# Kernel tuning notes

Hardware: AMD Instinct MI355X
Metric: run time of the kernel (lower is better)

Reference implementation:

```python
import jax, jax.numpy as jnp
import numpy as np

EPS = 1e-5  # BatchNorm2d eps
NEG_SLOPE = 0.01  # LeakyReLU default


def _cconv_bn_act(x, W, b, g, beta):
    # Complex 1x1 conv + per-part BatchNorm (batch stats) + LeakyReLU.
    # x: [B,2,C,F,T]; W: [2,C,C] (real, imag); b, g, beta: [2,C]
    xr, xi = x[:, 0], x[:, 1]
    yr = (jnp.einsum('oc,bcft->boft', W[0], xr)
          - jnp.einsum('oc,bcft->boft', W[1], xi) + b[0][None, :, None, None])
    yi = (jnp.einsum('oc,bcft->boft', W[0], xi)
          + jnp.einsum('oc,bcft->boft', W[1], xr) + b[1][None, :, None, None])

    def bn(y, gg, bb):
        mu = y.mean(axis=(0, 2, 3), keepdims=True)
        var = y.var(axis=(0, 2, 3), keepdims=True)  # biased, as torch BN normalization
        return (y - mu) / jnp.sqrt(var + EPS) * gg[None, :, None, None] + bb[None, :, None, None]

    yr = jax.nn.leaky_relu(bn(yr, g[0], beta[0]), NEG_SLOPE)
    yi = jax.nn.leaky_relu(bn(yi, g[1], beta[1]), NEG_SLOPE)
    return jnp.stack((yr, yi), axis=1)


def _complex_attn(q, k, v):
    # q,k,v: [B,2,N,D]; magnitude-based scores, softmax over dim=1 of [B,N,N]
    # (faithful to nn.Softmax(dim=1) applied to a 3-D score tensor).
    qr, qi = q[:, 0], q[:, 1]
    kr, ki = k[:, 0], k[:, 1]
    sr = jnp.einsum('bnd,bmd->bnm', qr, kr) + jnp.einsum('bnd,bmd->bnm', qi, ki)
    si = jnp.einsum('bnd,bmd->bnm', qi, kr) - jnp.einsum('bnd,bmd->bnm', qr, ki)
    a = jax.nn.softmax(jnp.sqrt(sr * sr + si * si), axis=1)
    outr = jnp.einsum('bnm,bmd->bnd', a, v[:, 0])
    outi = jnp.einsum('bnm,bmd->bnd', a, v[:, 1])
    return jnp.stack((outr, outi), axis=1)


def _forward(P, Q, W, b, g, beta):
    B, _, C, F, T = P.shape
    # --- Time-axis attention: tokens = T frames, feature dim = C*F ---
    qt = _cconv_bn_act(Q, W[0], b[0], g[0], beta[0])
    kt = _cconv_bn_act(P, W[1], b[1], g[1], beta[1])
    vt = _cconv_bn_act(P, W[2], b[2], g[2], beta[2])

    def to_time(x):  # [B,2,C,F,T] -> [B,2,T,C*F]
        return x.reshape(B, 2, C * F, T).transpose(0, 1, 3, 2)

    ot = _complex_attn(to_time(qt), to_time(kt), to_time(vt))
    ot = ot.transpose(0, 1, 3, 2).reshape(B, 2, C, F, T)

    # --- Freq-axis attention: tokens = F bins, feature dim = C*T ---
    qf = _cconv_bn_act(Q, W[3], b[3], g[3], beta[3])
    kf = _cconv_bn_act(P, W[4], b[4], g[4], beta[4])
    vf = _cconv_bn_act(P, W[5], b[5], g[5], beta[5])

    def to_freq(x):  # [B,2,C,F,T] -> [B,2,F,C*T]
        return x.transpose(0, 1, 3, 2, 4).reshape(B, 2, F, C * T)

    of = _complex_attn(to_freq(qf), to_freq(kf), to_freq(vf))
    of = of.reshape(B, 2, F, C, T).transpose(0, 1, 3, 2, 4)

    # Combine the two attention axes (truncated top-level module; see notes).
    return ot + of


def setup_inputs():
    key = jax.random.key(0)
    ks = jax.random.split(key, 4)
    B, C, F, T = 2, 64, 256, 256
    P = jax.random.normal(ks[0], (B, 2, C, F, T), dtype=jnp.float32)
    Q = jax.random.normal(ks[1], (B, 2, C, F, T), dtype=jnp.float32)
    # 6 branches: [time-q, time-k, time-v, freq-q, freq-k, freq-v]
    W = jax.random.normal(ks[2], (6, 2, C, C), dtype=jnp.float32) / np.sqrt(C).astype(np.float32)
    b = jax.random.normal(ks[3], (6, 2, C), dtype=jnp.float32) * 0.01
    g = jnp.ones((6, 2, C), dtype=jnp.float32)
    beta = jnp.zeros((6, 2, C), dtype=jnp.float32)
    return {"P": P, "Q": Q, "W": W, "b": b, "g": g, "beta": beta}


def reference(P, Q, W, b, g, beta):
    return _forward(P, Q, W, b, g, beta)
```

## Files before the change

kernel.cpp:

```cpp
#include <hip/hip_runtime.h>
#include <math.h>

#define SS 65536
#define PLANE 4194304
#define TEN_ELEMS 16777216
#define NSAMP 131072.0f

typedef __bf16 bf16x8 __attribute__((ext_vector_type(8)));
typedef __bf16 bf16x4v __attribute__((ext_vector_type(4)));
typedef float  f32x4  __attribute__((ext_vector_type(4)));

__device__ inline f32x4 mfma16(bf16x8 a, bf16x8 b, f32x4 c) {
  return __builtin_amdgcn_mfma_f32_16x16x32_bf16(a, b, c, 0, 0, 0);
}
__device__ inline bf16x8 neg8(bf16x8 v) {
  union { bf16x8 b; unsigned u[4]; } t; t.b = v;
#pragma unroll
  for (int i = 0; i < 4; ++i) t.u[i] ^= 0x80008000u;
  return t.b;
}
__device__ inline float bnlrelu(float v, float sc, float sh) {
  float t = fmaf(v, sc, sh);
  return t > 0.f ? t : 0.01f * t;
}

__device__ inline int swz(int r, int g) {
  return r * 40 + (((g ^ (r >> 2) ^ (r >> 4)) & 3) << 3);
}

__global__ __launch_bounds__(256) void stats_cov(
    const float* __restrict__ xQ, const float* __restrict__ xP,
    float* __restrict__ cpart, float* __restrict__ mbuck)
{
  __shared__ __align__(16) __bf16 sXh[128 * 72];
  __shared__ __align__(16) __bf16 sXl[128 * 72];
  const int tid = threadIdx.x;
  const int win = blockIdx.x;
  const int tz = blockIdx.y;
  const float* x = tz ? xP : xQ;
  const int w = tid >> 6, q = (tid >> 4) & 3, ln = tid & 15;
  const int pcb = tid >> 4;
  const int s4 = (tid & 15) * 4;

  f32x4 zero = {0.f, 0.f, 0.f, 0.f};
  f32x4 acc[2][8];
#pragma unroll
  for (int mt = 0; mt < 2; ++mt)
#pragma unroll
    for (int nt = 0; nt < 8; ++nt) acc[mt][nt] = zero;
  float msum[8] = {0.f, 0.f, 0.f, 0.f, 0.f, 0.f, 0.f, 0.f};

  for (int half = 0; half < 8; ++half) {
    const int bb = half >> 2;
    const int sbase = win * 256 + (half & 3) * 64;
#pragma unroll
    for (int r = 0; r < 8; ++r) {
      int pc = pcb + r * 16;
      float4 v4 = *(const float4*)&x[(size_t)(bb * 128 + pc) * SS + sbase + s4];
      msum[r] += v4.x + v4.y + v4.z + v4.w;
      float vv[4] = {v4.x, v4.y, v4.z, v4.w};
      bf16x4v hv, lv;
#pragma unroll
      for (int e = 0; e < 4; ++e) {
        __bf16 h = (__bf16)vv[e];
        hv[e] = h; lv[e] = (__bf16)(vv[e] - (float)h);
      }
      *(bf16x4v*)&sXh[pc * 72 + s4] = hv;
      *(bf16x4v*)&sXl[pc * 72 + s4] = lv;
    }
    __syncthreads();
#pragma unroll
    for (int ks = 0; ks < 2; ++ks) {
      bf16x8 ah[2], al[2];
#pragma unroll
      for (int mt = 0; mt < 2; ++mt) {
        int ra = w * 32 + mt * 16 + ln;
        ah[mt] = *(const bf16x8*)&sXh[ra * 72 + ks * 32 + q * 8];
        al[mt] = *(const bf16x8*)&sXl[ra * 72 + ks * 32 + q * 8];
      }
#pragma unroll
      for (int nt = 0; nt < 8; ++nt) {
        int rb = nt * 16 + ln;
        bf16x8 bh = *(const bf16x8*)&sXh[rb * 72 + ks * 32 + q * 8];
        bf16x8 bl = *(const bf16x8*)&sXl[rb * 72 + ks * 32 + q * 8];
#pragma unroll
        for (int mt = 0; mt < 2; ++mt) {
          f32x4 a = acc[mt][nt];
          a = mfma16(ah[mt], bh, a);
          a = mfma16(ah[mt], bl, a);
          a = mfma16(al[mt], bh, a);
          acc[mt][nt] = a;
        }
      }
    }
    __syncthreads();
  }
#pragma unroll
  for (int r = 0; r < 8; ++r) {
    float v = msum[r];
#pragma unroll
    for (int off = 1; off < 16; off <<= 1) v += __shfl_xor(v, off, 64);
    if (ln == 0)
      atomicAdd(&mbuck[((win & 63) * 2 + tz) * 128 + pcb + r * 16], v);
  }
  float* cp = cpart + ((size_t)tz * 256 + win) * 16384;
#pragma unroll
  for (int mt = 0; mt < 2; ++mt)
#pragma unroll
    for (int nt = 0; nt < 8; ++nt)
#pragma unroll
      for (int r = 0; r < 4; ++r) {
        int row = w * 32 + mt * 16 + q * 4 + r;
        int col = nt * 16 + ln;
        cp[row * 128 + col] = acc[mt][nt][r];
      }
}

__global__ __launch_bounds__(256) void cov_reduce(
    const float* __restrict__ cpart, const float* __restrict__ mbuck,
    float* __restrict__ csum, float* __restrict__ msum)
{
  int i = blockIdx.x * 256 + threadIdx.x;
  int tz = i >> 14, e = i & 16383;
  const float* p = cpart + (size_t)tz * 256 * 16384 + e;
  float s = 0.f;
#pragma unroll 4
  for (int k = 0; k < 256; ++k) s += p[(size_t)k * 16384];
  csum[i] = s;
  if (i < 256) {
    int t2 = i >> 7, row = i & 127;
    float sm2 = 0.f;
#pragma unroll 4
    for (int k = 0; k < 64; ++k) sm2 += mbuck[(k * 2 + t2) * 128 + row];
    msum[i] = sm2;
  }
}

__global__ void bn_precompute(
    const float* __restrict__ Cq, const float* __restrict__ Cp,
    const float* __restrict__ mq, const float* __restrict__ mp,
    const float* __restrict__ W, const float* __restrict__ g,
    const float* __restrict__ beta,
    float* __restrict__ scale6, float* __restrict__ shift6)
{
  const int rr = blockIdx.x >> 7;
  const int o  = blockIdx.x & 127;
  const int i  = threadIdx.x;
  const float* C = (rr % 3 == 0) ? Cq : Cp;
  const float* m = (rr % 3 == 0) ? mq : mp;
  const int po = o >> 6, co = o & 63;
  const int pi = i >> 6, ci = i & 63;
  float wv = W[rr * 8192 + ((po ^ pi) << 12) + co * 64 + ci];
  if (po == 0 && pi == 1) wv = -wv;
  __shared__ float sW[128];
  sW[i] = wv;
  __syncthreads();
  float t = 0.f;
  const float* crow = C + i * 128;
#pragma unroll 8
  for (int j = 0; j < 128; ++j) t += crow[j] * sW[j];
  float pv = wv * t;
  float pm = wv * m[i];
#pragma unroll
  for (int off = 1; off < 64; off <<= 1) {
    pv += __shfl_xor(pv, off, 64);
    pm += __shfl_xor(pm, off, 64);
  }
  __shared__ float red[4];
  if ((i & 63) == 0) { red[(i >> 6) * 2] = pv; red[(i >> 6) * 2 + 1] = pm; }
  __syncthreads();
  if (i == 0) {
    float v = red[0] + red[2];
    float wm = red[1] + red[3];
    float muT = wm / NSAMP;
    float var = v / NSAMP - muT * muT;
    float sc = g[rr * 128 + o] * rsqrtf(var + 1e-5f);
    scale6[rr * 128 + o] = sc;
    shift6[rr * 128 + o] = beta[rr * 128 + o] - muT * sc;
  }
}

__global__ __launch_bounds__(256) void cconv_mfma(
    const float* __restrict__ x, const float* __restrict__ Wj,
    const float* __restrict__ scale, const float* __restrict__ shiftp,
    void* __restrict__ outA, void* __restrict__ outB, int mode, int freq)
{
  __shared__ __align__(16) char smemBlk[34816];
  __bf16* sBh = (__bf16*)smemBlk;
  __bf16* sBl = (__bf16*)(smemBlk + 17408);
  const int tid = threadIdx.x;
  const int b = blockIdx.y;
  const int s0 = blockIdx.x << 6;
  const int w = tid >> 6, q = (tid >> 4) & 3, ln = tid & 15;

  bf16x8 ah[2][4], al[2][4];
#pragma unroll
  for (int mt = 0; mt < 2; ++mt) {
    int row = w * 32 + mt * 16 + ln;
    int po = row >> 6, co = row & 63;
#pragma unroll
    for (int ks = 0; ks < 4; ++ks) {
      bf16x8 vh, vl;
#pragma unroll
      for (int j = 0; j < 8; ++j) {
        int k = ks * 32 + q * 8 + j;
        int pi = k >> 6, c = k & 63;
        float v = Wj[((po ^ pi) << 12) + co * 64 + c];
        if (po == 0 && pi == 1) v = -v;
        __bf16 h = (__bf16)v;
        vh[j] = h;
        vl[j] = (__bf16)(v - (float)h);
      }
      ah[mt][ks] = vh; al[mt][ks] = vl;
    }
  }

#pragma unroll
  for (int ph = 0; ph < 2; ++ph) {
    int pc = ph * 64 + (tid & 63);
    const float* rowp = x + (size_t)(b * 128 + pc) * SS + s0;
#pragma unroll
    for (int sh2 = 0; sh2 < 2; ++sh2)
#pragma unroll
      for (int sc2 = 0; sc2 < 2; ++sc2) {
        int sl = ((tid >> 6) << 3) + sh2 * 32 + sc2 * 4;
        float4 rd = *(const float4*)&rowp[sl];
        float vv[4] = {rd.x, rd.y, rd.z, rd.w};
#pragma unroll
        for (int e = 0; e < 4; ++e) {
          __bf16 h = (__bf16)vv[e];
          sBh[(sl + e) * 136 + pc] = h;
          sBl[(sl + e) * 136 + pc] = (__bf16)(vv[e] - (float)h);
        }
      }
  }
  __syncthreads();

  f32x4 zero = {0.f, 0.f, 0.f, 0.f};
  f32x4 acc[2][4];
#pragma unroll
  for (int mt = 0; mt < 2; ++mt)
#pragma unroll
    for (int nt = 0; nt < 4; ++nt) acc[mt][nt] = zero;

#pragma unroll
  for (int ks = 0; ks < 4; ++ks) {
    bf16x8 bh[4], bl[4];
#pragma unroll
    for (int nt = 0; nt < 4; ++nt) {
      int off = (nt * 16 + ln) * 136 + ks * 32 + q * 8;
      bh[nt] = *(const bf16x8*)&sBh[off];
      bl[nt] = *(const bf16x8*)&sBl[off];
    }
#pragma unroll
    for (int mt = 0; mt < 2; ++mt)
#pragma unroll
      for (int nt = 0; nt < 4; ++nt) {
        acc[mt][nt] = mfma16(ah[mt][ks], bh[nt], acc[mt][nt]);
        acc[mt][nt] = mfma16(ah[mt][ks], bl[nt], acc[mt][nt]);
        acc[mt][nt] = mfma16(al[mt][ks], bh[nt], acc[mt][nt]);
      }
  }

  float scv[2][4], shv[2][4];
#pragma unroll
  for (int mt = 0; mt < 2; ++mt)
#pragma unroll
    for (int r = 0; r < 4; ++r) {
      int row = w * 32 + mt * 16 + q * 4 + r;
      scv[mt][r] = scale[row];
      shv[mt][r] = shiftp[row];
    }

  if (mode == 2) {
    float* y = (float*)outA;
#pragma unroll
    for (int mt = 0; mt < 2; ++mt)
#pragma unroll
      for (int r = 0; r < 4; ++r) {
        int row = w * 32 + mt * 16 + q * 4 + r;
#pragma unroll
        for (int nt = 0; nt < 4; ++nt)
          y[(size_t)(b * 128 + row) * SS + s0 + nt * 16 + ln] =
              bnlrelu(acc[mt][nt][r], scv[mt][r], shv[mt][r]);
      }
  } else if (mode == 1) {
    __bf16* vh = (__bf16*)outA;
    __bf16* vl = (__bf16*)outB;
    const int f = s0 >> 8, t0 = s0 & 255;
#pragma unroll
    for (int mt = 0; mt < 2; ++mt)
#pragma unroll
      for (int r = 0; r < 4; ++r) {
        int row = w * 32 + mt * 16 + q * 4 + r;
        int p = row >> 6, c = row & 63;
        size_t rbase = ((size_t)((b * 2 + p) * 16384 + c * 256 + f)) * 256 + t0;
#pragma unroll
        for (int nt = 0; nt < 4; ++nt) {
          float v = bnlrelu(acc[mt][nt][r], scv[mt][r], shv[mt][r]);
          __bf16 h = (__bf16)v;
          vh[rbase + nt * 16 + ln] = h;
          vl[rbase + nt * 16 + ln] = (__bf16)(v - (float)h);
        }
      }
  } else {
    __syncthreads();
    float* sT = (float*)smemBlk;
#pragma unroll
    for (int mt = 0; mt < 2; ++mt)
#pragma unroll
      for (int nt = 0; nt < 4; ++nt)
#pragma unroll
        for (int r = 0; r < 4; ++r)
          sT[(nt * 16 + ln) * 133 + (w * 32 + mt * 16 + q * 4 + r)] =
              bnlrelu(acc[mt][nt][r], scv[mt][r], shv[mt][r]);
    __syncthreads();
    const int pch = tid >> 6, tl = tid & 63;
    float vv[32];
#pragma unroll
    for (int j2 = 0; j2 < 8; ++j2)
      *(f32x4*)&vv[j2 * 4] = *(const f32x4*)&sT[tl * 133 + pch * 32 + j2 * 4];
    bf16x8 hh[4], ll[4];
#pragma unroll
    for (int j2 = 0; j2 < 4; ++j2)
#pragma unroll
      for (int e = 0; e < 8; ++e) {
        float v = vv[j2 * 8 + e];
        __bf16 h = (__bf16)v;
        hh[j2][e] = h; ll[j2][e] = (__bf16)(v - (float)h);
      }
    __bf16* out = (__bf16*)outA;
    if (!freq) {
      const int p = pch >> 1, ch2 = pch & 1;
      int chunk = (s0 >> 8) * 2 + ch2;
      int tok = (s0 & 255) + tl;
      size_t a = (size_t)(b * 2 + p) * (2 * (size_t)PLANE) +
                 ((size_t)chunk * 256 + tok) * 64;
#pragma unroll
      for (int j2 = 0; j2 < 4; ++j2) {
        *(bf16x8*)&out[a + j2 * 8]      = hh[j2];
        *(bf16x8*)&out[a + 32 + j2 * 8] = ll[j2];
      }
    } else {
      __syncthreads();
      __bf16* sP = (__bf16*)smemBlk;
      __bf16* me = sP + tid * 64;
#pragma unroll
      for (int j2 = 0; j2 < 4; ++j2) {
        *(bf16x8*)&me[j2 * 8]      = hh[j2];
        *(bf16x8*)&me[32 + j2 * 8] = ll[j2];
      }
      __syncthreads();
#pragma unroll
      for (int r2 = 0; r2 < 8; ++r2) {
        int u = tid + (r2 << 8);
        int g2 = u >> 3, piece = u & 7;
        int pch2 = g2 >> 6, t2 = g2 & 63;
        int chunk = ((s0 & 255) + t2) * 2 + (pch2 & 1);
        int tok = s0 >> 8;
        size_t a = (size_t)(b * 2 + (pch2 >> 1)) * (2 * (size_t)PLANE) +
                   ((size_t)chunk * 256 + tok) * 64 + piece * 8;
        *(bf16x8*)&out[a] = *(const bf16x8*)&sP[(size_t)u * 8];
      }
    }
  }
}

__global__ __launch_bounds__(256) void score_mfma(
    const __bf16* __restrict__ qt, const __bf16* __restrict__ kt,
    float* __restrict__ SR, float* __restrict__ SI)
{
  __shared__ __align__(16) __bf16 sQh[2 * 128 * 40], sQl[2 * 128 * 40];
  __shared__ __align__(16) __bf16 sKh[2 * 64 * 40],  sKl[2 * 64 * 40];
  const int tid = threadIdx.x;
  const int sid = blockIdx.x + (blockIdx.y << 3) + (blockIdx.z << 8);
  const int kk = sid & 7, tt = sid >> 3;
  const int n0 = (kk & 1) << 7;
  const int b  = (kk >> 1) & 1;
  const int m0 = (tt & 3) << 6;
  const int g0 = (((kk >> 2) << 4) + (tt >> 2)) << 4;
  const int w = tid >> 6, q4 = (tid >> 4) & 3, ln = tid & 15;
  const size_t pb = (size_t)(b * 2) * (2 * (size_t)PLANE);

  f32x4 zero = {0.f, 0.f, 0.f, 0.f};
  f32x4 accr[2][4], acci[2][4];
#pragma unroll
  for (int st = 0; st < 2; ++st)
#pragma unroll
    for (int mt = 0; mt < 4; ++mt) { accr[st][mt] = zero; acci[st][mt] = zero; }

  for (int ch = 0; ch < 16; ++ch) {
    const int g = g0 + ch;
    const int Gq = g * 256 + n0;
    const int Gk = g * 256 + m0;
#pragma unroll
    for (int r = 0; r < 4; ++r) {
      int u = tid + (r << 8);
      int g_ = u & 3, tok = (u >> 2) & 127, p = u >> 9;
      size_t a = pb + (size_t)p * (2 * (size_t)PLANE) +
                 (size_t)(Gq + tok) * 64 + (g_ << 3);
      int dst = swz(p * 128 + tok, g_);
      *(bf16x8*)&sQh[dst] = *(const bf16x8*)&qt[a];
      *(bf16x8*)&sQl[dst] = *(const bf16x8*)&qt[a + 32];
    }
#pragma unroll
    for (int r = 0; r < 2; ++r) {
      int u = tid + (r << 8);
      int g_ = u & 3, tok = (u >> 2) & 63, p = u >> 8;
      size_t a = pb + (size_t)p * (2 * (size_t)PLANE) +
                 (size_t)(Gk + tok) * 64 + (g_ << 3);
      int dst = swz(p * 64 + tok, g_);
      *(bf16x8*)&sKh[dst] = *(const bf16x8*)&kt[a];
      *(bf16x8*)&sKl[dst] = *(const bf16x8*)&kt[a + 32];
    }
    __syncthreads();

    bf16x8 qh[2][2], ql2[2][2], nqh[2], nql[2];
#pragma unroll
    for (int st = 0; st < 2; ++st) {
      int tokn = w * 32 + st * 16 + ln;
#pragma unroll
      for (int p = 0; p < 2; ++p) {
        int off = swz(p * 128 + tokn, q4);
        qh[st][p]  = *(const bf16x8*)&sQh[off];
        ql2[st][p] = *(const bf16x8*)&sQl[off];
      }
      nqh[st] = neg8(qh[st][0]);
      nql[st] = neg8(ql2[st][0]);
    }
#pragma unroll
    for (int mt = 0; mt < 4; ++mt) {
      int tk = mt * 16 + ln;
      int offr = swz(tk, q4), offi = swz(64 + tk, q4);
      bf16x8 krh = *(const bf16x8*)&sKh[offr];
      bf16x8 krl = *(const bf16x8*)&sKl[offr];
      bf16x8 kih = *(const bf16x8*)&sKh[offi];
      bf16x8 kil = *(const bf16x8*)&sKl[offi];
#pragma unroll
      for (int st = 0; st < 2; ++st) {
        f32x4 ar = accr[st][mt], ai = acci[st][mt];
        ar = mfma16(qh[st][0], krh, ar);
        ar = mfma16(qh[st][0], krl, ar);
        ar = mfma16(ql2[st][0], krh, ar);
        ar = mfma16(qh[st][1], kih, ar);
        ar = mfma16(qh[st][1], kil, ar);
        ar = mfma16(ql2[st][1], kih, ar);
        ai = mfma16(qh[st][1], krh, ai);
        ai = mfma16(qh[st][1], krl, ai);
        ai = mfma16(ql2[st][1], krh, ai);
        ai = mfma16(nqh[st], kih, ai);
        ai = mfma16(nqh[st], kil, ai);
        ai = mfma16(nql[st], kih, ai);
        accr[st][mt] = ar; acci[st][mt] = ai;
      }
    }
    __syncthreads();
  }

#pragma unroll
  for (int st = 0; st < 2; ++st)
#pragma unroll
    for (int mt = 0; mt < 4; ++mt)
#pragma unroll
      for (int r = 0; r < 4; ++r) {
        int n = n0 + w * 32 + st * 16 + q4 * 4 + r;
        int m = m0 + mt * 16 + ln;
        int idx = (b << 16) + (n << 8) + m;
        atomicAdd(&SR[idx], accr[st][mt][r]);
        atomicAdd(&SI[idx], acci[st][mt][r]);
      }
}

__global__ __launch_bounds__(256) void softmax_kernel(
    const float* __restrict__ sr, const float* __restrict__ si,
    float* __restrict__ am)
{
  const int m = blockIdx.x & 255;
  const int b = blockIdx.x >> 8;
  const int n = threadIdx.x;
  const int idx = (b << 16) + (n << 8) + m;
  float vr = sr[idx], vi = si[idx];
  float mag = sqrtf(vr * vr + vi * vi);
  __shared__ float wmax[4];
  __shared__ float wsum[4];
  float mx = mag;
  #pragma unroll
  for (int off = 1; off < 64; off <<= 1)
    mx = fmaxf(mx, __shfl_xor(mx, off, 64));
  if ((threadIdx.x & 63) == 0) wmax[threadIdx.x >> 6] = mx;
  __syncthreads();
  mx = fmaxf(fmaxf(wmax[0], wmax[1]), fmaxf(wmax[2], wmax[3]));
  float e = expf(mag - mx);
  float sm = e;
  #pragma unroll
  for (int off = 1; off < 64; off <<= 1)
    sm += __shfl_xor(sm, off, 64);
  if ((threadIdx.x & 63) == 0) wsum[threadIdx.x >> 6] = sm;
  __syncthreads();
  float tot = wsum[0] + wsum[1] + wsum[2] + wsum[3];
  am[idx] = e / tot;
}

__global__ __launch_bounds__(256) void vt_transpose(
    const float* __restrict__ y2, __bf16* __restrict__ vh,
    __bf16* __restrict__ vl)
{
  __shared__ float sT[64 * 65];
  const int tid = threadIdx.x;
  const int bpc = blockIdx.y;
  const int bp = bpc >> 6, c = bpc & 63;
  const int f0 = (blockIdx.x >> 2) << 6, t0 = (blockIdx.x & 3) << 6;
  const float* src = y2 + (size_t)bp * PLANE + (size_t)c * SS;
#pragma unroll
  for (int r = 0; r < 4; ++r) {
    int fl = (tid >> 4) + (r << 4);
    int tl = (tid & 15) << 2;
    float4 v = *(const float4*)&src[(f0 + fl) * 256 + t0 + tl];
    sT[fl * 65 + tl + 0] = v.x;
    sT[fl * 65 + tl + 1] = v.y;
    sT[fl * 65 + tl + 2] = v.z;
    sT[fl * 65 + tl + 3] = v.w;
  }
  __syncthreads();
  __bf16* dsth = vh + (((size_t)bp * 16384 + c * 256) << 8);
  __bf16* dstl = vl + (((size_t)bp * 16384 + c * 256) << 8);
#pragma unroll
  for (int r = 0; r < 4; ++r) {
    int tl = (tid >> 4) + (r << 4);
    int fl = (tid & 15) << 2;
    bf16x4v h, l;
#pragma unroll
    for (int e = 0; e < 4; ++e) {
      float vv = sT[(fl + e) * 65 + tl];
      __bf16 hh = (__bf16)vv;
      h[e] = hh; l[e] = (__bf16)(vv - (float)hh);
    }
    *(bf16x4v*)&dsth[(size_t)(t0 + tl) * 256 + f0 + fl] = h;
    *(bf16x4v*)&dstl[(size_t)(t0 + tl) * 256 + f0 + fl] = l;
  }
}

__global__ __launch_bounds__(256) void av_mfma(
    const float* __restrict__ am, const __bf16* __restrict__ vth,
    const __bf16* __restrict__ vtl, float* __restrict__ out, int freq)
{
  __shared__ __align__(16) char smem[55296];
  __bf16* sVh = (__bf16*)smem;
  __bf16* sVl = (__bf16*)(smem + 18432);
  __bf16* sAh = (__bf16*)(smem + 36864);
  __bf16* sAl = (__bf16*)(smem + 46080);
  const int tid = threadIdx.x;
  const int d0 = blockIdx.x << 7;
  const int n0 = blockIdx.y << 6;
  const int bp = blockIdx.z, b = bp >> 1;
  const int w = tid >> 6, q = (tid >> 4) & 3, ln = tid & 15;
  const __bf16* vhp = vth + (((size_t)bp * 16384 + d0) << 8);
  const __bf16* vlp = vtl + (((size_t)bp * 16384 + d0) << 8);
  float* op = out + (size_t)bp * PLANE;

  f32x4 zero = {0.f, 0.f, 0.f, 0.f};
  f32x4 acc[2][4];
#pragma unroll
  for (int mt = 0; mt < 2; ++mt)
#pragma unroll
    for (int nt = 0; nt < 4; ++nt) acc[mt][nt] = zero;

  for (int m0 = 0; m0 < 256; m0 += 64) {
#pragma unroll
    for (int r = 0; r < 4; ++r) {
      int u = tid + (r << 8);
      int dl = u >> 3, g = (u & 7) << 3;
      *(bf16x8*)&sVh[dl * 72 + g] = *(const bf16x8*)&vhp[dl * 256 + m0 + g];
      *(bf16x8*)&sVl[dl * 72 + g] = *(const bf16x8*)&vlp[dl * 256 + m0 + g];
    }
#pragma unroll
    for (int r = 0; r < 4; ++r) {
      int u = tid + (r << 8);
      int mj = (u & 15) << 2, nl = u >> 4;
      float4 v4 = *(const float4*)&am[(b << 16) + ((n0 + nl) << 8) + m0 + mj];
      float vv[4] = {v4.x, v4.y, v4.z, v4.w};
      bf16x4v h, l;
#pragma unroll
      for (int e = 0; e < 4; ++e) {
        __bf16 hh = (__bf16)vv[e];
        h[e] = hh; l[e] = (__bf16)(vv[e] - (float)hh);
      }
      *(bf16x4v*)&sAh[nl * 72 + mj] = h;
      *(bf16x4v*)&sAl[nl * 72 + mj] = l;
    }
    __syncthreads();

#pragma unroll
    for (int ks = 0; ks < 2; ++ks) {
      bf16x8 vhf[2], vlf[2], ahf[4], alf[4];
#pragma unroll
      for (int mt = 0; mt < 2; ++mt) {
        int off = (w * 32 + mt * 16 + ln) * 72 + ks * 32 + q * 8;
        vhf[mt] = *(const bf16x8*)&sVh[off];
        vlf[mt] = *(const bf16x8*)&sVl[off];
      }
#pragma unroll
      for (int nt = 0; nt < 4; ++nt) {
        int off = (nt * 16 + ln) * 72 + ks * 32 + q * 8;
        ahf[nt] = *(const bf16x8*)&sAh[off];
        alf[nt] = *(const bf16x8*)&sAl[off];
      }
#pragma unroll
      for (int mt = 0; mt < 2; ++mt)
#pragma unroll
        for (int nt = 0; nt < 4; ++nt) {
          f32x4 a = acc[mt][nt];
          a = mfma16(vhf[mt], ahf[nt], a);
          a = mfma16(vhf[mt], alf[nt], a);
          a = mfma16(vlf[mt], ahf[nt], a);
          acc[mt][nt] = a;
        }
    }
    __syncthreads();
  }

  if (!freq) {
#pragma unroll
    for (int mt = 0; mt < 2; ++mt)
#pragma unroll
      for (int nt = 0; nt < 4; ++nt)
#pragma unroll
        for (int r = 0; r < 4; ++r) {
          int row = d0 + w * 32 + mt * 16 + q * 4 + r;
          op[(size_t)row * 256 + n0 + nt * 16 + ln] = acc[mt][nt][r];
        }
  } else {
    float* sO = (float*)smem;
#pragma unroll
    for (int mt = 0; mt < 2; ++mt)
#pragma unroll
      for (int nt = 0; nt < 4; ++nt)
#pragma unroll
        for (int r = 0; r < 4; ++r)
          sO[(w * 32 + mt * 16 + q * 4 + r) * 65 + nt * 16 + ln] = acc[mt][nt][r];
    __syncthreads();
    const int c = d0 >> 8, t0 = d0 & 255;
    const int dl = (tid & 31) << 2, nb = tid >> 5;
#pragma unroll
    for (int r = 0; r < 8; ++r) {
      int n = nb + (r << 3);
      float4 wv = make_float4(sO[(dl + 0) * 65 + n], sO[(dl + 1) * 65 + n],
                              sO[(dl + 2) * 65 + n], sO[(dl + 3) * 65 + n]);
      size_t addr = (size_t)c * SS + (size_t)(n0 + n) * 256 + t0 + dl;
      float4 o = *(float4*)&op[addr];
      wv.x += o.x; wv.y += o.y; wv.z += o.z; wv.w += o.w;
      *(float4*)&op[addr] = wv;
    }
  }
}

extern "C" void kernel_launch(void* const* d_in, const int* in_sizes, int n_in,
                              void* d_out, int out_size, void* d_ws, size_t ws_size,
                              hipStream_t stream) {
  const float* P    = (const float*)d_in[0];
  const float* Q    = (const float*)d_in[1];
  const float* W    = (const float*)d_in[2];
  const float* g    = (const float*)d_in[4];
  const float* beta = (const float*)d_in[5];
  float* out = (float*)d_out;
  float* ws  = (float*)d_ws;

  float* Y0    = ws;
  float* Y1    = Y0 + TEN_ELEMS;
  float* Y2    = Y1 + TEN_ELEMS;
  float* SR    = Y2 + TEN_ELEMS;
  float* SI    = SR + 131072;
  float* AM    = SI + 131072;
  float* MBUCK = AM + 131072;
  float* CSUM  = MBUCK + 16384;
  float* MSUM  = CSUM + 32768;
  float* SCALE6 = MSUM + 256;
  float* SHIFT6 = SCALE6 + 768;

  hipMemsetAsync(MBUCK, 0, 16384 * sizeof(float), stream);
  stats_cov<<<dim3(256, 2), 256, 0, stream>>>(Q, P, Y2, MBUCK);
  cov_reduce<<<128, 256, 0, stream>>>(Y2, MBUCK, CSUM, MSUM);
  bn_precompute<<<768, 128, 0, stream>>>(CSUM, CSUM + 16384, MSUM, MSUM + 128,
                                         W, g, beta, SCALE6, SHIFT6);

  for (int phase = 0; phase < 2; ++phase) {
    int j0 = phase * 3;
    int freq = phase;
    cconv_mfma<<<dim3(1024, 2), 256, 0, stream>>>(
        Q, W + (size_t)j0 * 8192, SCALE6 + j0 * 128, SHIFT6 + j0 * 128,
        Y0, nullptr, 0, freq);
    cconv_mfma<<<dim3(1024, 2), 256, 0, stream>>>(
        P, W + (size_t)(j0 + 1) * 8192, SCALE6 + (j0 + 1) * 128,
        SHIFT6 + (j0 + 1) * 128, Y1, nullptr, 0, freq);
    if (!freq)
      cconv_mfma<<<dim3(1024, 2), 256, 0, stream>>>(
          P, W + (size_t)(j0 + 2) * 8192, SCALE6 + (j0 + 2) * 128,
          SHIFT6 + (j0 + 2) * 128, Y2, (char*)Y2 + (size_t)TEN_ELEMS * 2, 1, 0);
    else
      cconv_mfma<<<dim3(1024, 2), 256, 0, stream>>>(
          P, W + (size_t)(j0 + 2) * 8192, SCALE6 + (j0 + 2) * 128,
          SHIFT6 + (j0 + 2) * 128, Y2, nullptr, 2, 1);

    hipMemsetAsync(SR, 0, 2 * 131072 * sizeof(float), stream);
    score_mfma<<<dim3(8, 32, 2), 256, 0, stream>>>(
        (const __bf16*)Y0, (const __bf16*)Y1, SR, SI);
    softmax_kernel<<<512, 256, 0, stream>>>(SR, SI, AM);

    const __bf16* VTh;
    const __bf16* VTl;
    if (!freq) {
      VTh = (const __bf16*)Y2;
      VTl = (const __bf16*)((char*)Y2 + (size_t)TEN_ELEMS * 2);
    } else {
      vt_transpose<<<dim3(16, 256), 256, 0, stream>>>(
          Y2, (__bf16*)Y0, (__bf16*)((char*)Y0 + (size_t)TEN_ELEMS * 2));
      VTh = (const __bf16*)Y0;
      VTl = (const __bf16*)((char*)Y0 + (size_t)TEN_ELEMS * 2);
    }
    av_mfma<<<dim3(128, 4, 4), 256, 0, stream>>>(AM, VTh, VTl, out, freq);
  }
}
```

Before: 741.4 us.

## Fuse K and V complex convs sharing P tile; register-prefetch score loads

Adds a cconv_kv kernel that loads and splits each P tile into bf16 hi/lo in shared memory once, then computes both the K and V projections from it. This replaces two separate conv launches that each re-read P, and mode flags are removed from cconv_mfma. Separately, score_mfma now precomputes its load addresses and prefetches the next chunk's Q/K tiles into registers while the current chunk is computed, to hide global load latency. Both kernels hold more accumulators and registers live at once, which may lower occupancy.

```diff
diff --git a/kernel.cpp b/kernel.cpp
--- a/kernel.cpp
+++ b/kernel.cpp
@@ -183,7 +183,7 @@
 __global__ __launch_bounds__(256) void cconv_mfma(
     const float* __restrict__ x, const float* __restrict__ Wj,
     const float* __restrict__ scale, const float* __restrict__ shiftp,
-    void* __restrict__ outA, void* __restrict__ outB, int mode, int freq)
+    void* __restrict__ outA, int freq)
 {
   __shared__ __align__(16) char smemBlk[34816];
   __bf16* sBh = (__bf16*)smemBlk;
@@ -272,21 +272,171 @@
       shv[mt][r] = shiftp[row];
     }
 
-  if (mode == 2) {
-    float* y = (float*)outA;
+  __syncthreads();
+  float* sT = (float*)smemBlk;
+#pragma unroll
+  for (int mt = 0; mt < 2; ++mt)
+#pragma unroll
+    for (int nt = 0; nt < 4; ++nt)
+#pragma unroll
+      for (int r = 0; r < 4; ++r)
+        sT[(nt * 16 + ln) * 133 + (w * 32 + mt * 16 + q * 4 + r)] =
+            bnlrelu(acc[mt][nt][r], scv[mt][r], shv[mt][r]);
+  __syncthreads();
+  const int pch = tid >> 6, tl = tid & 63;
+  float vv[32];
+#pragma unroll
+  for (int j2 = 0; j2 < 8; ++j2)
+    *(f32x4*)&vv[j2 * 4] = *(const f32x4*)&sT[tl * 133 + pch * 32 + j2 * 4];
+  bf16x8 hh[4], ll[4];
+#pragma unroll
+  for (int j2 = 0; j2 < 4; ++j2)
+#pragma unroll
+    for (int e = 0; e < 8; ++e) {
+      float v = vv[j2 * 8 + e];
+      __bf16 h = (__bf16)v;
+      hh[j2][e] = h; ll[j2][e] = (__bf16)(v - (float)h);
+    }
+  __bf16* out = (__bf16*)outA;
+  if (!freq) {
+    const int p = pch >> 1, ch2 = pch & 1;
+    int chunk = (s0 >> 8) * 2 + ch2;
+    int tok = (s0 & 255) + tl;
+    size_t a = (size_t)(b * 2 + p) * (2 * (size_t)PLANE) +
+               ((size_t)chunk * 256 + tok) * 64;
+#pragma unroll
+    for (int j2 = 0; j2 < 4; ++j2) {
+      *(bf16x8*)&out[a + j2 * 8]      = hh[j2];
+      *(bf16x8*)&out[a + 32 + j2 * 8] = ll[j2];
+    }
+  } else {
+    __syncthreads();
+    __bf16* sP = (__bf16*)smemBlk;
+    __bf16* me = sP + tid * 64;
+#pragma unroll
+    for (int j2 = 0; j2 < 4; ++j2) {
+      *(bf16x8*)&me[j2 * 8]      = hh[j2];
+      *(bf16x8*)&me[32 + j2 * 8] = ll[j2];
+    }
+    __syncthreads();
+#pragma unroll
+    for (int r2 = 0; r2 < 8; ++r2) {
+      int u = tid + (r2 << 8);
+      int g2 = u >> 3, piece = u & 7;
+      int pch2 = g2 >> 6, t2 = g2 & 63;
+      int chunk = ((s0 & 255) + t2) * 2 + (pch2 & 1);
+      int tok = s0 >> 8;
+      size_t a = (size_t)(b * 2 + (pch2 >> 1)) * (2 * (size_t)PLANE) +
+                 ((size_t)chunk * 256 + tok) * 64 + piece * 8;
+      *(bf16x8*)&out[a] = *(const bf16x8*)&sP[(size_t)u * 8];
+    }
+  }
+}
+
+__global__ __launch_bounds__(256) void cconv_kv(
+    const float* __restrict__ x,
+    const float* __restrict__ Wk, const float* __restrict__ Wv,
+    const float* __restrict__ scK, const float* __restrict__ shK,
+    const float* __restrict__ scV, const float* __restrict__ shV,
+    void* __restrict__ outK, void* __restrict__ outVa,
+    void* __restrict__ outVb, int freq)
+{
+  __shared__ __align__(16) char smemBlk[34816];
+  __bf16* sBh = (__bf16*)smemBlk;
+  __bf16* sBl = (__bf16*)(smemBlk + 17408);
+  const int tid = threadIdx.x;
+  const int b = blockIdx.y;
+  const int s0 = blockIdx.x << 6;
+  const int w = tid >> 6, q = (tid >> 4) & 3, ln = tid & 15;
+
+#pragma unroll
+  for (int ph = 0; ph < 2; ++ph) {
+    int pc = ph * 64 + (tid & 63);
+    const float* rowp = x + (size_t)(b * 128 + pc) * SS + s0;
+#pragma unroll
+    for (int sh2 = 0; sh2 < 2; ++sh2)
+#pragma unroll
+      for (int sc2 = 0; sc2 < 2; ++sc2) {
+        int sl = ((tid >> 6) << 3) + sh2 * 32 + sc2 * 4;
+        float4 rd = *(const float4*)&rowp[sl];
+        float vv[4] = {rd.x, rd.y, rd.z, rd.w};
+#pragma unroll
+        for (int e = 0; e < 4; ++e) {
+          __bf16 h = (__bf16)vv[e];
+          sBh[(sl + e) * 136 + pc] = h;
+          sBl[(sl + e) * 136 + pc] = (__bf16)(vv[e] - (float)h);
+        }
+      }
+  }
+  __syncthreads();
+
+  f32x4 zero = {0.f, 0.f, 0.f, 0.f};
+  f32x4 accKV[2][2][4];
+#pragma unroll
+  for (int role = 0; role < 2; ++role)
 #pragma unroll
     for (int mt = 0; mt < 2; ++mt)
 #pragma unroll
-      for (int r = 0; r < 4; ++r) {
-        int row = w * 32 + mt * 16 + q * 4 + r;
-#pragma unroll
-        for (int nt = 0; nt < 4; ++nt)
-          y[(size_t)(b * 128 + row) * SS + s0 + nt * 16 + ln] =
-              bnlrelu(acc[mt][nt][r], scv[mt][r], shv[mt][r]);
-      }
-  } else if (mode == 1) {
-    __bf16* vh = (__bf16*)outA;
-    __bf16* vl = (__bf16*)outB;
+      for (int nt = 0; nt < 4; ++nt) accKV[role][mt][nt] = zero;
+
+  for (int role = 0; role < 2; ++role) {
+    const float* Wj = role ? Wv : Wk;
+    bf16x8 ah[2][4], al[2][4];
+#pragma unroll
+    for (int mt = 0; mt < 2; ++mt) {
+      int row = w * 32 + mt * 16 + ln;
+      int po = row >> 6, co = row & 63;
+#pragma unroll
+      for (int ks = 0; ks < 4; ++ks) {
+        bf16x8 vh, vl;
+#pragma unroll
+        for (int j = 0; j < 8; ++j) {
+          int k = ks * 32 + q * 8 + j;
+          int pi = k >> 6, c = k & 63;
+          float v = Wj[((po ^ pi) << 12) + co * 64 + c];
+          if (po == 0 && pi == 1) v = -v;
+          __bf16 h = (__bf16)v;
+          vh[j] = h;
+          vl[j] = (__bf16)(v - (float)h);
+        }
+        ah[mt][ks] = vh; al[mt][ks] = vl;
+      }
+    }
+#pragma unroll
+    for (int ks = 0; ks < 4; ++ks) {
+      bf16x8 bh[4], bl[4];
+#pragma unroll
+      for (int nt = 0; nt < 4; ++nt) {
+        int off = (nt * 16 + ln) * 136 + ks * 32 + q * 8;
+        bh[nt] = *(const bf16x8*)&sBh[off];
+        bl[nt] = *(const bf16x8*)&sBl[off];
+      }
+#pragma unroll
+      for (int mt = 0; mt < 2; ++mt)
+#pragma unroll
+        for (int nt = 0; nt < 4; ++nt) {
+          f32x4 a = accKV[role][mt][nt];
+          a = mfma16(ah[mt][ks], bh[nt], a);
+          a = mfma16(ah[mt][ks], bl[nt], a);
+          a = mfma16(al[mt][ks], bh[nt], a);
+          accKV[role][mt][nt] = a;
+        }
+    }
+  }
+
+  float scvK[2][4], shvK[2][4], scvV[2][4], shvV[2][4];
+#pragma unroll
+  for (int mt = 0; mt < 2; ++mt)
+#pragma unroll
+    for (int r = 0; r < 4; ++r) {
+      int row = w * 32 + mt * 16 + q * 4 + r;
+      scvK[mt][r] = scK[row]; shvK[mt][r] = shK[row];
+      scvV[mt][r] = scV[row]; shvV[mt][r] = shV[row];
+    }
+
+  if (!freq) {
+    __bf16* vh = (__bf16*)outVa;
+    __bf16* vl = (__bf16*)outVb;
     const int f = s0 >> 8, t0 = s0 & 255;
 #pragma unroll
     for (int mt = 0; mt < 2; ++mt)
@@ -297,71 +447,83 @@
         size_t rbase = ((size_t)((b * 2 + p) * 16384 + c * 256 + f)) * 256 + t0;
 #pragma unroll
         for (int nt = 0; nt < 4; ++nt) {
-          float v = bnlrelu(acc[mt][nt][r], scv[mt][r], shv[mt][r]);
+          float v = bnlrelu(accKV[1][mt][nt][r], scvV[mt][r], shvV[mt][r]);
           __bf16 h = (__bf16)v;
           vh[rbase + nt * 16 + ln] = h;
           vl[rbase + nt * 16 + ln] = (__bf16)(v - (float)h);
         }
       }
   } else {
-    __syncthreads();
-    float* sT = (float*)smemBlk;
+    float* y = (float*)outVa;
 #pragma unroll
     for (int mt = 0; mt < 2; ++mt)
 #pragma unroll
-      for (int nt = 0; nt < 4; ++nt)
-#pragma unroll
-        for (int r = 0; r < 4; ++r)
-          sT[(nt * 16 + ln) * 133 + (w * 32 + mt * 16 + q * 4 + r)] =
-              bnlrelu(acc[mt][nt][r], scv[mt][r], shv[mt][r]);
-    __syncthreads();
-    const int pch = tid >> 6, tl = tid & 63;
-    float vv[32];
-#pragma unroll
-    for (int j2 = 0; j2 < 8; ++j2)
-      *(f32x4*)&vv[j2 * 4] = *(const f32x4*)&sT[tl * 133 + pch * 32 + j2 * 4];
-    bf16x8 hh[4], ll[4];
-#pragma unroll
-    for (int j2 = 0; j2 < 4; ++j2)
-#pragma unroll
-      for (int e = 0; e < 8; ++e) {
-        float v = vv[j2 * 8 + e];
-        __bf16 h = (__bf16)v;
-        hh[j2][e] = h; ll[j2][e] = (__bf16)(v - (float)h);
-      }
-    __bf16* out = (__bf16*)outA;
-    if (!freq) {
-      const int p = pch >> 1, ch2 = pch & 1;
-      int chunk = (s0 >> 8) * 2 + ch2;
-      int tok = (s0 & 255) + tl;
-      size_t a = (size_t)(b * 2 + p) * (2 * (size_t)PLANE) +
-                 ((size_t)chunk * 256 + tok) * 64;
-#pragma unroll
-      for (int j2 = 0; j2 < 4; ++j2) {
-        *(bf16x8*)&out[a + j2 * 8]      = hh[j2];
-        *(bf16x8*)&out[a + 32 + j2 * 8] = ll[j2];
-      }
-    } else {
-      __syncthreads();
-      __bf16* sP = (__bf16*)smemBlk;
-      __bf16* me = sP + tid * 64;
-#pragma unroll
-      for (int j2 = 0; j2 < 4; ++j2) {
-        *(bf16x8*)&me[j2 * 8]      = hh[j2];
-        *(bf16x8*)&me[32 + j2 * 8] = ll[j2];
-      }
-      __syncthreads();
-#pragma unroll
-      for (int r2 = 0; r2 < 8; ++r2) {
-        int u = tid + (r2 << 8);
-        int g2 = u >> 3, piece = u & 7;
-        int pch2 = g2 >> 6, t2 = g2 & 63;
-        int chunk = ((s0 & 255) + t2) * 2 + (pch2 & 1);
-        int tok = s0 >> 8;
-        size_t a = (size_t)(b * 2 + (pch2 >> 1)) * (2 * (size_t)PLANE) +
-                   ((size_t)chunk * 256 + tok) * 64 + piece * 8;
-        *(bf16x8*)&out[a] = *(const bf16x8*)&sP[(size_t)u * 8];
-      }
+      for (int r = 0; r < 4; ++r) {
+        int row = w * 32 + mt * 16 + q * 4 + r;
+#pragma unroll
+        for (int nt = 0; nt < 4; ++nt)
+          y[(size_t)(b * 128 + row) * SS + s0 + nt * 16 + ln] =
+              bnlrelu(accKV[1][mt][nt][r], scvV[mt][r], shvV[mt][r]);
+      }
+  }
+
+  __syncthreads();
+  float* sT = (float*)smemBlk;
+#pragma unroll
+  for (int mt = 0; mt < 2; ++mt)
+#pragma unroll
+    for (int nt = 0; nt < 4; ++nt)
+#pragma unroll
+      for (int r = 0; r < 4; ++r)
+        sT[(nt * 16 + ln) * 133 + (w * 32 + mt * 16 + q * 4 + r)] =
+            bnlrelu(accKV[0][mt][nt][r], scvK[mt][r], shvK[mt][r]);
+  __syncthreads();
+  const int pch = tid >> 6, tl = tid & 63;
+  float vv[32];
+#pragma unroll
+  for (int j2 = 0; j2 < 8; ++j2)
+    *(f32x4*)&vv[j2 * 4] = *(const f32x4*)&sT[tl * 133 + pch * 32 + j2 * 4];
+  bf16x8 hh[4], ll[4];
+#pragma unroll
+  for (int j2 = 0; j2 < 4; ++j2)
+#pragma unroll
+    for (int e = 0; e < 8; ++e) {
+      float v = vv[j2 * 8 + e];
+      __bf16 h = (__bf16)v;
+      hh[j2][e] = h; ll[j2][e] = (__bf16)(v - (float)h);
+    }
+  __bf16* out = (__bf16*)outK;
+  if (!freq) {
+    const int p = pch >> 1, ch2 = pch & 1;
+    int chunk = (s0 >> 8) * 2 + ch2;
+    int tok = (s0 & 255) + tl;
+    size_t a = (size_t)(b * 2 + p) * (2 * (size_t)PLANE) +
+               ((size_t)chunk * 256 + tok) * 64;
+#pragma unroll
+    for (int j2 = 0; j2 < 4; ++j2) {
+      *(bf16x8*)&out[a + j2 * 8]      = hh[j2];
+      *(bf16x8*)&out[a + 32 + j2 * 8] = ll[j2];
+    }
+  } else {
+    __syncthreads();
+    __bf16* sP = (__bf16*)smemBlk;
+    __bf16* me = sP + tid * 64;
+#pragma unroll
+    for (int j2 = 0; j2 < 4; ++j2) {
+      *(bf16x8*)&me[j2 * 8]      = hh[j2];
+      *(bf16x8*)&me[32 + j2 * 8] = ll[j2];
+    }
+    __syncthreads();
+#pragma unroll
+    for (int r2 = 0; r2 < 8; ++r2) {
+      int u = tid + (r2 << 8);
+      int g2 = u >> 3, piece = u & 7;
+      int pch2 = g2 >> 6, t2 = g2 & 63;
+      int chunk = ((s0 & 255) + t2) * 2 + (pch2 & 1);
+      int tok = s0 >> 8;
+      size_t a = (size_t)(b * 2 + (pch2 >> 1)) * (2 * (size_t)PLANE) +
+                 ((size_t)chunk * 256 + tok) * 64 + piece * 8;
+      *(bf16x8*)&out[a] = *(const bf16x8*)&sP[(size_t)u * 8];
     }
   }
 }
@@ -382,6 +544,25 @@
   const int w = tid >> 6, q4 = (tid >> 4) & 3, ln = tid & 15;
   const size_t pb = (size_t)(b * 2) * (2 * (size_t)PLANE);
 
+  size_t aq[4], ak[2];
+  int dq[4], dk[2];
+#pragma unroll
+  for (int r = 0; r < 4; ++r) {
+    int u = tid + (r << 8);
+    int g_ = u & 3, tok = (u >> 2) & 127, p = u >> 9;
+    aq[r] = pb + (size_t)p * (2 * (size_t)PLANE) +
+            (size_t)(g0 * 256 + n0 + tok) * 64 + (g_ << 3);
+    dq[r] = swz(p * 128 + tok, g_);
+  }
+#pragma unroll
+  for (int r = 0; r < 2; ++r) {
+    int u = tid + (r << 8);
+    int g_ = u & 3, tok = (u >> 2) & 63, p = u >> 8;
+    ak[r] = pb + (size_t)p * (2 * (size_t)PLANE) +
+            (size_t)(g0 * 256 + m0 + tok) * 64 + (g_ << 3);
+    dk[r] = swz(p * 64 + tok, g_);
+  }
+
   f32x4 zero = {0.f, 0.f, 0.f, 0.f};
   f32x4 accr[2][4], acci[2][4];
 #pragma unroll
@@ -389,29 +570,41 @@
 #pragma unroll
     for (int mt = 0; mt < 4; ++mt) { accr[st][mt] = zero; acci[st][mt] = zero; }
 
+  bf16x8 pqh[4], pql[4], pkh[2], pkl[2];
+#pragma unroll
+  for (int r = 0; r < 4; ++r) {
+    pqh[r] = *(const bf16x8*)&qt[aq[r]];
+    pql[r] = *(const bf16x8*)&qt[aq[r] + 32];
+  }
+#pragma unroll
+  for (int r = 0; r < 2; ++r) {
+    pkh[r] = *(const bf16x8*)&kt[ak[r]];
+    pkl[r] = *(const bf16x8*)&kt[ak[r] + 32];
+  }
+
   for (int ch = 0; ch < 16; ++ch) {
-    const int g = g0 + ch;
-    const int Gq = g * 256 + n0;
-    const int Gk = g * 256 + m0;
 #pragma unroll
     for (int r = 0; r < 4; ++r) {
-      int u = tid + (r << 8);
-      int g_ = u & 3, tok = (u >> 2) & 127, p = u >> 9;
-      size_t a = pb + (size_t)p * (2 * (size_t)PLANE) +
-                 (size_t)(Gq + tok) * 64 + (g_ << 3);
-      int dst = swz(p * 128 + tok, g_);
-      *(bf16x8*)&sQh[dst] = *(const bf16x8*)&qt[a];
-      *(bf16x8*)&sQl[dst] = *(const bf16x8*)&qt[a + 32];
+      *(bf16x8*)&sQh[dq[r]] = pqh[r];
+      *(bf16x8*)&sQl[dq[r]] = pql[r];
     }
 #pragma unroll
     for (int r = 0; r < 2; ++r) {
-      int u = tid + (r << 8);
-      int g_ = u & 3, tok = (u >> 2) & 63, p = u >> 8;
-      size_t a = pb + (size_t)p * (2 * (size_t)PLANE) +
-                 (size_t)(Gk + tok) * 64 + (g_ << 3);
-      int dst = swz(p * 64 + tok, g_);
-      *(bf16x8*)&sKh[dst] = *(const bf16x8*)&kt[a];
-      *(bf16x8*)&sKl[dst] = *(const bf16x8*)&kt[a + 32];
+      *(bf16x8*)&sKh[dk[r]] = pkh[r];
+      *(bf16x8*)&sKl[dk[r]] = pkl[r];
+    }
+    if (ch < 15) {
+      size_t d = (size_t)(ch + 1) * 16384;
+#pragma unroll
+      for (int r = 0; r < 4; ++r) {
+        pqh[r] = *(const bf16x8*)&qt[aq[r] + d];
+        pql[r] = *(const bf16x8*)&qt[aq[r] + d + 32];
+      }
+#pragma unroll
+      for (int r = 0; r < 2; ++r) {
+        pkh[r] = *(const bf16x8*)&kt[ak[r] + d];
+        pkl[r] = *(const bf16x8*)&kt[ak[r] + d + 32];
+      }
     }
     __syncthreads();
 
@@ -688,18 +881,13 @@
     int freq = phase;
     cconv_mfma<<<dim3(1024, 2), 256, 0, stream>>>(
         Q, W + (size_t)j0 * 8192, SCALE6 + j0 * 128, SHIFT6 + j0 * 128,
-        Y0, nullptr, 0, freq);
-    cconv_mfma<<<dim3(1024, 2), 256, 0, stream>>>(
-        P, W + (size_t)(j0 + 1) * 8192, SCALE6 + (j0 + 1) * 128,
-        SHIFT6 + (j0 + 1) * 128, Y1, nullptr, 0, freq);
-    if (!freq)
-      cconv_mfma<<<dim3(1024, 2), 256, 0, stream>>>(
-          P, W + (size_t)(j0 + 2) * 8192, SCALE6 + (j0 + 2) * 128,
-          SHIFT6 + (j0 + 2) * 128, Y2, (char*)Y2 + (size_t)TEN_ELEMS * 2, 1, 0);
-    else
-      cconv_mfma<<<dim3(1024, 2), 256, 0, stream>>>(
-          P, W + (size_t)(j0 + 2) * 8192, SCALE6 + (j0 + 2) * 128,
-          SHIFT6 + (j0 + 2) * 128, Y2, nullptr, 2, 1);
+        Y0, freq);
+    cconv_kv<<<dim3(1024, 2), 256, 0, stream>>>(
+        P, W + (size_t)(j0 + 1) * 8192, W + (size_t)(j0 + 2) * 8192,
+        SCALE6 + (j0 + 1) * 128, SHIFT6 + (j0 + 1) * 128,
+        SCALE6 + (j0 + 2) * 128, SHIFT6 + (j0 + 2) * 128,
+        Y1, Y2, freq ? nullptr : (void*)((char*)Y2 + (size_t)TEN_ELEMS * 2),
+        freq);
 
     hipMemsetAsync(SR, 0, 2 * 131072 * sizeof(float), stream);
     score_mfma<<<dim3(8, 32, 2), 256, 0, stream>>>(
```

Measured after the change: 742.7 us. About the same (+0.2%).
